# Performance work log

Measured on AMD Instinct MI355X. Metric: run time of the kernel, lower is better.

The kernel has to match this reference:

```python
import jax, jax.numpy as jnp
import numpy as np

B, T, D = 64, 128, 1024
E = 2048      # embedding_dim of state encoder
CD = 256      # VQ code_dim
NC = 1024     # num_codes
BETA = 0.25   # commitment cost


def setup_inputs() -> dict:
    key = jax.random.key(0)
    ks = jax.random.split(key, 5)
    states = jax.random.normal(ks[0], (B, T, D), dtype=jnp.float32)
    next_states = jax.random.normal(ks[1], (B, T, D), dtype=jnp.float32)
    # VarianceScaling(scale=2.0, fan_in) init
    W_s = jax.random.normal(ks[2], (D, E), dtype=jnp.float32) * np.sqrt(2.0 / D)
    b_s = jnp.zeros((E,), dtype=jnp.float32)
    W_p = jax.random.normal(ks[3], (2 * E, CD), dtype=jnp.float32) * np.sqrt(2.0 / (2 * E))
    b_p = jnp.zeros((CD,), dtype=jnp.float32)
    codebook = jax.random.normal(ks[4], (NC, CD), dtype=jnp.float32)
    return {"states": states, "next_states": next_states, "W_s": W_s,
            "b_s": b_s, "W_p": W_p, "b_p": b_p, "codebook": codebook}


def reference(states, next_states, W_s, b_s, W_p, b_p, codebook):
    # dual state encoder (shared weights)
    se = states @ W_s + b_s            # (B,T,E)
    ne = next_states @ W_s + b_s       # (B,T,E)
    policy_input = jax.nn.gelu(jnp.concatenate([se, ne], axis=-1))  # (B,T,2E)
    latent = policy_input @ W_p + b_p  # (B,T,CD)

    # --- VectorQuantizerEMA forward ---
    flat = latent.reshape(-1, CD)      # (N, CD), N = B*T
    # squared euclidean distances to codebook rows
    dists = (jnp.sum(flat * flat, axis=1, keepdims=True)
             - 2.0 * flat @ codebook.T
             + jnp.sum(codebook * codebook, axis=1))  # (N, NC)
    idx = jnp.argmin(dists, axis=1)                    # (N,)
    encodings = jax.nn.one_hot(idx, NC, dtype=latent.dtype)  # (N, NC)
    quantize = codebook[idx].reshape(latent.shape)     # (B,T,CD)

    e_latent_loss = jnp.mean(jnp.square(jax.lax.stop_gradient(quantize) - latent))
    loss = BETA * e_latent_loss
    # straight-through estimator
    quantize_st = latent + jax.lax.stop_gradient(quantize - latent)

    avg_probs = jnp.mean(encodings, axis=0)
    perplexity = jnp.exp(-jnp.sum(avg_probs * jnp.log(avg_probs + 1e-10)))

    encodings = encodings.reshape(B, T, NC)
    encoding_indices = idx.reshape(B, T)
    return quantize_st, loss, perplexity, encodings, encoding_indices
```

## Files before the change

kernel.cpp:

```cpp
#include <hip/hip_runtime.h>

#define NROW  8192
#define D_    1024
#define E_    2048
#define P2E_  4096
#define CD_   256
#define NC_   1024
#define BETA_ 0.25f

typedef __attribute__((ext_vector_type(8))) short short8;
typedef __attribute__((ext_vector_type(4))) float f32x4;

__device__ __forceinline__ ushort f2bf(float x) {
    union { float f; unsigned u; } v; v.f = x;
    unsigned r = (v.u + 0x7fffu + ((v.u >> 16) & 1u)) >> 16;
    return (ushort)r;
}
__device__ __forceinline__ float bf2f(ushort h) {
    union { unsigned u; float f; } v; v.u = ((unsigned)h) << 16;
    return v.f;
}
__device__ __forceinline__ void split2(float x, ushort& h, ushort& l) {
    h = f2bf(x);
    l = f2bf(x - bf2f(h));
}
__device__ __forceinline__ float gelu_tanh(float x) {
    float x3 = x * x * x;
    return 0.5f * x * (1.0f + tanhf(0.7978845608028654f * (x + 0.044715f * x3)));
}

#define GLD16(gp, lp) __builtin_amdgcn_global_load_lds( \
    (const __attribute__((address_space(1))) void*)(gp), \
    (__attribute__((address_space(3))) void*)(lp), 16, 0, 0)

template<int EPI>
__global__ __launch_bounds__(256)
void gemm_bf16x3(const ushort* __restrict__ Ah, const ushort* __restrict__ Al,
                 const ushort* __restrict__ Bh, const ushort* __restrict__ Bl,
                 int K, int ksteps,
                 const float* __restrict__ bias,
                 float* __restrict__ outF,
                 ushort* __restrict__ oPh, ushort* __restrict__ oPl,
                 const float* __restrict__ rn, const float* __restrict__ cn)
{
    __shared__ alignas(16) ushort sAh[4096], sAl[4096], sBh[4096], sBl[4096];
    const int t = threadIdx.x;
    const int l = t & 63;
    const int w = t >> 6;
    const int wr = w >> 1, wc = w & 1;
    const int bm = blockIdx.y * 128;
    const int bn = blockIdx.x * 128;
    const int kstart = (EPI == 1) ? (int)blockIdx.z * (ksteps * 32) : 0;

    const int srow = t >> 2;
    const int scol = (t & 3) * 8;
    const ushort* gAh = Ah + (size_t)(bm + srow) * K + kstart + scol;
    const ushort* gAl = Al + (size_t)(bm + srow) * K + kstart + scol;
    const ushort* gBh = Bh + (size_t)(bn + srow) * K + kstart + scol;
    const ushort* gBl = Bl + (size_t)(bn + srow) * K + kstart + scol;
    const size_t rstep = (size_t)64 * K;
    const int lo0 = t * 8, lo1 = t * 8 + 2048;

    f32x4 acc[4][4];
#pragma unroll
    for (int i = 0; i < 4; i++)
#pragma unroll
        for (int j = 0; j < 4; j++) acc[i][j] = (f32x4)0.0f;

    const int ar = (wr * 64 + (l & 15)) * 32 + (l >> 4) * 8;
    const int br = (wc * 64 + (l & 15)) * 32 + (l >> 4) * 8;

    for (int s = 0; s < ksteps; ++s) {
        GLD16(gAh, &sAh[lo0]); GLD16(gAh + rstep, &sAh[lo1]);
        GLD16(gAl, &sAl[lo0]); GLD16(gAl + rstep, &sAl[lo1]);
        GLD16(gBh, &sBh[lo0]); GLD16(gBh + rstep, &sBh[lo1]);
        GLD16(gBl, &sBl[lo0]); GLD16(gBl + rstep, &sBl[lo1]);
        __syncthreads();

        short8 fah[4], fal[4], fbh[4], fbl[4];
#pragma unroll
        for (int i = 0; i < 4; i++) {
            fah[i] = *(const short8*)&sAh[ar + i * 16 * 32];
            fal[i] = *(const short8*)&sAl[ar + i * 16 * 32];
            fbh[i] = *(const short8*)&sBh[br + i * 16 * 32];
            fbl[i] = *(const short8*)&sBl[br + i * 16 * 32];
        }
#pragma unroll
        for (int i = 0; i < 4; i++)
#pragma unroll
            for (int j = 0; j < 4; j++) {
                acc[i][j] = __builtin_amdgcn_mfma_f32_16x16x32_bf16(fah[i], fbh[j], acc[i][j], 0, 0, 0);
                acc[i][j] = __builtin_amdgcn_mfma_f32_16x16x32_bf16(fah[i], fbl[j], acc[i][j], 0, 0, 0);
                acc[i][j] = __builtin_amdgcn_mfma_f32_16x16x32_bf16(fal[i], fbh[j], acc[i][j], 0, 0, 0);
            }
        __syncthreads();
        gAh += 32; gAl += 32; gBh += 32; gBl += 32;
    }

#pragma unroll
    for (int i = 0; i < 4; i++) {
        const int grow = bm + wr * 64 + i * 16 + (l >> 4) * 4;
#pragma unroll
        for (int j = 0; j < 4; j++) {
            const int gcol = bn + wc * 64 + j * 16 + (l & 15);
            f32x4 a = acc[i][j];
            if constexpr (EPI == 0) {
                const float bb = bias[gcol];
#pragma unroll
                for (int r = 0; r < 4; r++) {
                    int m = grow + r;
                    float x = gelu_tanh(a[r] + bb);
                    ushort h, lo; split2(x, h, lo);
                    int pr = (m < NROW) ? m : m - NROW;
                    int pc = ((m < NROW) ? 0 : E_) + gcol;
                    oPh[(size_t)pr * P2E_ + pc] = h;
                    oPl[(size_t)pr * P2E_ + pc] = lo;
                }
            } else if constexpr (EPI == 1) {
                float* o = outF + ((size_t)NROW * blockIdx.z + grow) * CD_ + gcol;
#pragma unroll
                for (int r = 0; r < 4; r++) o[(size_t)r * CD_] = a[r];
            } else {
#pragma unroll
                for (int r = 0; r < 4; r++) {
                    int m = grow + r;
                    outF[(size_t)m * NC_ + gcol] = (rn[m] - 2.0f * a[r]) + cn[gcol];
                }
            }
        }
    }
}

__global__ void split_k(const float* __restrict__ in, ushort* __restrict__ oh,
                        ushort* __restrict__ ol, int n4)
{
    int i = blockIdx.x * blockDim.x + threadIdx.x;
    int stride = gridDim.x * blockDim.x;
    for (; i < n4; i += stride) {
        float4 v = ((const float4*)in)[i];
        ushort4 h, lo;
        split2(v.x, h.x, lo.x); split2(v.y, h.y, lo.y);
        split2(v.z, h.z, lo.z); split2(v.w, h.w, lo.w);
        ((ushort4*)oh)[i] = h;
        ((ushort4*)ol)[i] = lo;
    }
}

__global__ __launch_bounds__(1024)
void tsplit_k(const float* __restrict__ in, ushort* __restrict__ oh,
              ushort* __restrict__ ol, int R, int C)
{
    __shared__ float tile[32][33];
    int c0 = blockIdx.x * 32, r0 = blockIdx.y * 32;
    int tx = threadIdx.x, ty = threadIdx.y;
    tile[ty][tx] = in[(size_t)(r0 + ty) * C + c0 + tx];
    __syncthreads();
    float x = tile[tx][ty];
    ushort h, lo; split2(x, h, lo);
    size_t o = (size_t)(c0 + ty) * R + r0 + tx;
    oh[o] = h; ol[o] = lo;
}

__global__ __launch_bounds__(256)
void combine_k(const float* __restrict__ part, const float* __restrict__ bias,
               float* __restrict__ latent, ushort* __restrict__ lh,
               ushort* __restrict__ ll, float* __restrict__ rown)
{
    __shared__ float red[256];
    int row = blockIdx.x, t = threadIdx.x;
    float x = bias[t];
#pragma unroll
    for (int z = 0; z < 4; z++) x += part[((size_t)z * NROW + row) * CD_ + t];
    latent[(size_t)row * CD_ + t] = x;
    ushort h, lo; split2(x, h, lo);
    lh[(size_t)row * CD_ + t] = h;
    ll[(size_t)row * CD_ + t] = lo;
    red[t] = x * x;
    __syncthreads();
    for (int st = 128; st > 0; st >>= 1) { if (t < st) red[t] += red[t + st]; __syncthreads(); }
    if (t == 0) rown[row] = red[0];
}

__global__ __launch_bounds__(256) void row_norms(const float* __restrict__ X,
                                                 float* __restrict__ out)
{
    __shared__ float s[256];
    int n = blockIdx.x, t = threadIdx.x;
    float v = X[(size_t)n * 256 + t];
    s[t] = v * v;
    __syncthreads();
    for (int st = 128; st > 0; st >>= 1) {
        if (t < st) s[t] += s[t + st];
        __syncthreads();
    }
    if (t == 0) out[n] = s[0];
}

__global__ void zero_hist(int* hist) { hist[threadIdx.x] = 0; }

__global__ __launch_bounds__(256) void vq_kernel(
    const float* __restrict__ latent, const float* __restrict__ cb,
    float* __restrict__ dists_enc, float* __restrict__ out_q,
    float* __restrict__ out_idx, int* __restrict__ hist, float* __restrict__ lpart)
{
    __shared__ float sd[256];
    __shared__ int   si[256];
    const int n = blockIdx.x, tid = threadIdx.x;
    float* drow = dists_enc + (size_t)n * NC_;

    float best = INFINITY;
    int bidx = 0;
#pragma unroll
    for (int j = 0; j < NC_ / 256; j++) {
        int c = tid + j * 256;
        float d = drow[c];
        if (d < best) { best = d; bidx = c; }
    }
    sd[tid] = best; si[tid] = bidx;
    __syncthreads();
    for (int st = 128; st > 0; st >>= 1) {
        if (tid < st) {
            float d2 = sd[tid + st]; int i2 = si[tid + st];
            if (d2 < sd[tid] || (d2 == sd[tid] && i2 < si[tid])) { sd[tid] = d2; si[tid] = i2; }
        }
        __syncthreads();
    }
    const int bc = si[0];

#pragma unroll
    for (int j = 0; j < NC_ / 256; j++) {
        int c = tid + j * 256;
        drow[c] = (c == bc) ? 1.0f : 0.0f;
    }

    float lv = latent[(size_t)n * CD_ + tid];
    float q  = cb[(size_t)bc * CD_ + tid];
    out_q[(size_t)n * CD_ + tid] = lv + (q - lv);
    float diff = q - lv;
    __syncthreads();
    sd[tid] = diff * diff;
    __syncthreads();
    for (int st = 128; st > 0; st >>= 1) {
        if (tid < st) sd[tid] += sd[tid + st];
        __syncthreads();
    }
    if (tid == 0) {
        lpart[n] = sd[0];
        atomicAdd(&hist[bc], 1);
        out_idx[n] = (float)bc;
    }
}

__global__ __launch_bounds__(1024) void finalize_kernel(
    const float* __restrict__ lpart, const int* __restrict__ hist,
    float* __restrict__ out_loss, float* __restrict__ out_perp)
{
    __shared__ float s[1024];
    int t = threadIdx.x;
    float x = 0.0f;
    for (int i = t; i < NROW; i += 1024) x += lpart[i];
    s[t] = x;
    __syncthreads();
    for (int st = 512; st > 0; st >>= 1) {
        if (t < st) s[t] += s[t + st];
        __syncthreads();
    }
    float total = s[0];
    __syncthreads();
    float p = (float)hist[t] * (1.0f / NROW);
    s[t] = p * logf(p + 1e-10f);
    __syncthreads();
    for (int st = 512; st > 0; st >>= 1) {
        if (t < st) s[t] += s[t + st];
        __syncthreads();
    }
    if (t == 0) {
        *out_loss = BETA_ * (total / (float)((size_t)NROW * CD_));
        *out_perp = expf(-s[0]);
    }
}

extern "C" void kernel_launch(void* const* d_in, const int* in_sizes, int n_in,
                              void* d_out, int out_size, void* d_ws, size_t ws_size,
                              hipStream_t stream)
{
    const float* states      = (const float*)d_in[0];
    const float* next_states = (const float*)d_in[1];
    const float* W_s         = (const float*)d_in[2];
    const float* b_s         = (const float*)d_in[3];
    const float* W_p         = (const float*)d_in[4];
    const float* b_p         = (const float*)d_in[5];
    const float* codebook    = (const float*)d_in[6];

    float* out      = (float*)d_out;
    float* out_q    = out;
    float* out_loss = out + (size_t)NROW * CD_;
    float* out_perp = out_loss + 1;
    float* out_enc  = out_perp + 1;
    float* out_idx  = out_enc + (size_t)NROW * NC_;

    char* ws = (char*)d_ws;
    size_t off = 0;
    auto alloc = [&](size_t bytes) { void* p = ws + off; off += (bytes + 255) & ~255ull; return p; };

    ushort* A1h  = (ushort*)alloc((size_t)2 * NROW * D_ * 2);
    ushort* A1l  = (ushort*)alloc((size_t)2 * NROW * D_ * 2);
    ushort* WsTh = (ushort*)alloc((size_t)E_ * D_ * 2);
    ushort* WsTl = (ushort*)alloc((size_t)E_ * D_ * 2);
    ushort* WpTh = (ushort*)alloc((size_t)CD_ * P2E_ * 2);
    ushort* WpTl = (ushort*)alloc((size_t)CD_ * P2E_ * 2);
    ushort* cbh  = (ushort*)alloc((size_t)NC_ * CD_ * 2);
    ushort* cbl  = (ushort*)alloc((size_t)NC_ * CD_ * 2);
    ushort* Ph   = (ushort*)alloc((size_t)NROW * P2E_ * 2);
    ushort* Pl   = (ushort*)alloc((size_t)NROW * P2E_ * 2);
    ushort* lath = (ushort*)alloc((size_t)NROW * CD_ * 2);
    ushort* latl = (ushort*)alloc((size_t)NROW * CD_ * 2);
    float*  rown = (float*)alloc(NROW * 4);
    float*  cbn  = (float*)alloc(NC_ * 4);
    int*    hist = (int*)alloc(NC_ * 4);
    float*  lpart= (float*)alloc(NROW * 4);
    float* lat_part = (float*)A1h;
    float* latent   = (float*)WsTh;

    {
        int n4 = NROW * D_ / 4;
        split_k<<<2048, 256, 0, stream>>>(states, A1h, A1l, n4);
        split_k<<<2048, 256, 0, stream>>>(next_states, A1h + (size_t)NROW * D_,
                                          A1l + (size_t)NROW * D_, n4);
    }
    tsplit_k<<<dim3(E_ / 32, D_ / 32), dim3(32, 32), 0, stream>>>(W_s, WsTh, WsTl, D_, E_);
    tsplit_k<<<dim3(CD_ / 32, P2E_ / 32), dim3(32, 32), 0, stream>>>(W_p, WpTh, WpTl, P2E_, CD_);
    split_k<<<256, 256, 0, stream>>>(codebook, cbh, cbl, NC_ * CD_ / 4);
    row_norms<<<NC_, 256, 0, stream>>>(codebook, cbn);

    gemm_bf16x3<0><<<dim3(E_ / 128, 2 * NROW / 128), 256, 0, stream>>>(
        A1h, A1l, WsTh, WsTl, D_, D_ / 32, b_s, nullptr, Ph, Pl, nullptr, nullptr);

    gemm_bf16x3<1><<<dim3(CD_ / 128, NROW / 128, 4), 256, 0, stream>>>(
        Ph, Pl, WpTh, WpTl, P2E_, P2E_ / 32 / 4, nullptr, lat_part, nullptr, nullptr, nullptr, nullptr);

    combine_k<<<NROW, 256, 0, stream>>>(lat_part, b_p, latent, lath, latl, rown);

    gemm_bf16x3<2><<<dim3(NC_ / 128, NROW / 128), 256, 0, stream>>>(
        lath, latl, cbh, cbl, CD_, CD_ / 32, nullptr, out_enc, nullptr, nullptr, rown, cbn);

    zero_hist<<<1, NC_, 0, stream>>>(hist);
    vq_kernel<<<NROW, 256, 0, stream>>>(latent, codebook, out_enc, out_q, out_idx, hist, lpart);
    finalize_kernel<<<1, 1024, 0, stream>>>(lpart, hist, out_loss, out_perp);
}
```

Before: 409.6 us.

## Overlap global-to-LDS loads with MFMA, swizzle LDS and block order

Restructures the bf16x3 GEMM main loop so fragments are read from LDS into registers first, then the next k-step's global-to-LDS loads are issued before the MFMA work runs, letting memory traffic overlap compute. Adds an XOR swizzle on the LDS column layout (store and load sides) to reduce bank conflicts, remaps block IDs for better L2 locality, and raises wave priority around the MFMA block. The cost is an extra barrier per iteration, plus the risk that the swizzle or block remap is wrong for grids whose block count is not a multiple of 8.

```diff
diff --git a/kernel.cpp b/kernel.cpp
--- a/kernel.cpp
+++ b/kernel.cpp
@@ -48,12 +48,19 @@
     const int l = t & 63;
     const int w = t >> 6;
     const int wr = w >> 1, wc = w & 1;
-    const int bm = blockIdx.y * 128;
-    const int bn = blockIdx.x * 128;
+
+    const int nxy = gridDim.x * gridDim.y;
+    const int id  = blockIdx.y * gridDim.x + blockIdx.x;
+    const int swz = (id & 7) * (nxy >> 3) + (id >> 3);
+    const int bx  = swz % gridDim.x;
+    const int by  = swz / gridDim.x;
+
+    const int bm = by * 128;
+    const int bn = bx * 128;
     const int kstart = (EPI == 1) ? (int)blockIdx.z * (ksteps * 32) : 0;
 
     const int srow = t >> 2;
-    const int scol = (t & 3) * 8;
+    const int scol = ((t & 3) ^ ((t >> 3) & 3)) * 8;
     const ushort* gAh = Ah + (size_t)(bm + srow) * K + kstart + scol;
     const ushort* gAl = Al + (size_t)(bm + srow) * K + kstart + scol;
     const ushort* gBh = Bh + (size_t)(bn + srow) * K + kstart + scol;
@@ -67,16 +74,21 @@
 #pragma unroll
         for (int j = 0; j < 4; j++) acc[i][j] = (f32x4)0.0f;
 
-    const int ar = (wr * 64 + (l & 15)) * 32 + (l >> 4) * 8;
-    const int br = (wc * 64 + (l & 15)) * 32 + (l >> 4) * 8;
+    const int rsw = ((l >> 4) ^ (((l & 15) >> 1) & 3)) * 8;
+    const int ar = (wr * 64 + (l & 15)) * 32 + rsw;
+    const int br = (wc * 64 + (l & 15)) * 32 + rsw;
+
+#define STAGE8() do { \
+        GLD16(gAh, &sAh[lo0]); GLD16(gAh + rstep, &sAh[lo1]); \
+        GLD16(gAl, &sAl[lo0]); GLD16(gAl + rstep, &sAl[lo1]); \
+        GLD16(gBh, &sBh[lo0]); GLD16(gBh + rstep, &sBh[lo1]); \
+        GLD16(gBl, &sBl[lo0]); GLD16(gBl + rstep, &sBl[lo1]); \
+    } while (0)
+
+    STAGE8();
+    __syncthreads();
 
     for (int s = 0; s < ksteps; ++s) {
-        GLD16(gAh, &sAh[lo0]); GLD16(gAh + rstep, &sAh[lo1]);
-        GLD16(gAl, &sAl[lo0]); GLD16(gAl + rstep, &sAl[lo1]);
-        GLD16(gBh, &sBh[lo0]); GLD16(gBh + rstep, &sBh[lo1]);
-        GLD16(gBl, &sBl[lo0]); GLD16(gBl + rstep, &sBl[lo1]);
-        __syncthreads();
-
         short8 fah[4], fal[4], fbh[4], fbl[4];
 #pragma unroll
         for (int i = 0; i < 4; i++) {
@@ -85,6 +97,14 @@
             fbh[i] = *(const short8*)&sBh[br + i * 16 * 32];
             fbl[i] = *(const short8*)&sBl[br + i * 16 * 32];
         }
+        __syncthreads();
+
+        if (s + 1 < ksteps) {
+            gAh += 32; gAl += 32; gBh += 32; gBl += 32;
+            STAGE8();
+        }
+
+        __builtin_amdgcn_s_setprio(1);
 #pragma unroll
         for (int i = 0; i < 4; i++)
 #pragma unroll
@@ -93,9 +113,10 @@
                 acc[i][j] = __builtin_amdgcn_mfma_f32_16x16x32_bf16(fah[i], fbl[j], acc[i][j], 0, 0, 0);
                 acc[i][j] = __builtin_amdgcn_mfma_f32_16x16x32_bf16(fal[i], fbh[j], acc[i][j], 0, 0, 0);
             }
-        __syncthreads();
-        gAh += 32; gAl += 32; gBh += 32; gBl += 32;
-    }
+        __builtin_amdgcn_s_setprio(0);
+        __syncthreads();
+    }
+#undef STAGE8
 
 #pragma unroll
     for (int i = 0; i < 4; i++) {
```

New measurement: 346.2 us. 15.5% less time.
